# Optimization experiments

Measured on AMD Instinct MI355X. Metric: run time of the kernel, lower is better.

## Reference

```python
import jax, jax.numpy as jnp
import numpy as np

B, S, D, H = 2, 2048, 1024, 16
HD = D // H  # head dim = 64


def setup_inputs() -> dict:
    key = jax.random.key(0)
    ks = jax.random.split(key, 5)
    scale = 1.0 / np.sqrt(D)
    return {
        "hidden_states": jax.random.normal(ks[0], (B, S, D), jnp.float32),
        "attention_mask": jax.random.normal(ks[1], (B, 1, 1, S), jnp.float32),
        "Wq": jax.random.normal(ks[2], (D, D), jnp.float32) * scale,
        "bq": jnp.zeros((D,), jnp.float32),
        "Wk": jax.random.normal(ks[3], (D, D), jnp.float32) * scale,
        "bk": jnp.zeros((D,), jnp.float32),
        "Wv": jax.random.normal(ks[4], (D, D), jnp.float32) * scale,
        "bv": jnp.zeros((D,), jnp.float32),
    }


def _split_heads(x):
    # [B,S,D] -> [B,H,S,HD]
    return x.reshape(B, S, H, HD).transpose(0, 2, 1, 3)


def reference(hidden_states, attention_mask, Wq, bq, Wk, bk, Wv, bv):
    # torch Linear: y = x @ W.T + b
    q = _split_heads(hidden_states @ Wq.T + bq)
    k = _split_heads(hidden_states @ Wk.T + bk)
    v = _split_heads(hidden_states @ Wv.T + bv)

    scores = jnp.einsum("bhqd,bhkd->bhqk", q, k)
    # Faithful to source: with a mask present, the 1/sqrt(head_dim) scaling
    # is overwritten and raw scores are multiplied by the binary key mask.
    mask = (attention_mask >= 0).astype(scores.dtype)  # [B,1,1,S]
    probs = scores * mask
    # dropout prob = 0 (eval) -> identity

    ctx = jnp.einsum("bhqk,bhkd->bhqd", probs, v)
    ctx = ctx.transpose(0, 2, 1, 3).reshape(B, S, D)
    return ctx
```

## Files before the change

### kernel.cpp

```cpp
#include <hip/hip_runtime.h>

#define BB 2
#define SS 2048
#define DD 1024
#define HH 16
#define HDIM 64
#define MTOT 4096

typedef unsigned short u16;
typedef __bf16 bf16_t;
typedef bf16_t bf16x8 __attribute__((ext_vector_type(8)));
typedef float floatx4 __attribute__((ext_vector_type(4)));
typedef float floatx16 __attribute__((ext_vector_type(16)));

__device__ __forceinline__ float bf2f(u16 u) {
  union { unsigned int i; float f; } x;
  x.i = ((unsigned int)u) << 16;
  return x.f;
}
__device__ __forceinline__ u16 f2bf(float f) {
  union { float f; unsigned int i; } x;
  x.f = f;
  unsigned int r = x.i + 0x7fffu + ((x.i >> 16) & 1u);
  return (u16)(r >> 16);
}

__device__ __forceinline__ void gload16(const u16* g, u16* l) {
  __builtin_amdgcn_global_load_lds(
      (const __attribute__((address_space(1))) unsigned int*)g,
      (__attribute__((address_space(3))) unsigned int*)l, 16, 0, 0);
}

__global__ __launch_bounds__(256) void cast_to_bf16(
    const float* __restrict__ hs, const float* __restrict__ wq,
    const float* __restrict__ wk, const float* __restrict__ wv,
    u16* __restrict__ hs_b, u16* __restrict__ wq_b,
    u16* __restrict__ wk_b, u16* __restrict__ wv_b) {
  int fid = blockIdx.x * 256 + threadIdx.x;
  const float* src;
  u16* dst;
  int local;
  if (fid < 1048576) { src = hs; dst = hs_b; local = fid; }
  else if (fid < 1310720) { src = wq; dst = wq_b; local = fid - 1048576; }
  else if (fid < 1572864) { src = wk; dst = wk_b; local = fid - 1310720; }
  else { src = wv; dst = wv_b; local = fid - 1572864; }
  float4 v = reinterpret_cast<const float4*>(src)[local];
  ushort4 o;
  o.x = f2bf(v.x); o.y = f2bf(v.y); o.z = f2bf(v.z); o.w = f2bf(v.w);
  reinterpret_cast<ushort4*>(dst)[local] = o;
}

#define BKK 32
__global__ __launch_bounds__(256) void qkv_gemm_kernel(
    const u16* __restrict__ A,
    const u16* __restrict__ Wq, const u16* __restrict__ Wk, const u16* __restrict__ Wv,
    const float* __restrict__ bq, const float* __restrict__ bk, const float* __restrict__ bv,
    u16* __restrict__ Qo, u16* __restrict__ Ko, u16* __restrict__ Vo) {
  __shared__ u16 sA[128 * BKK];
  __shared__ u16 sB[128 * BKK];
  const int mt = blockIdx.y, ntall = blockIdx.x;
  const int seg = ntall >> 3, nt = ntall & 7;
  const u16* Wp = (seg == 0) ? Wq : (seg == 1) ? Wk : Wv;
  const float* bp = (seg == 0) ? bq : (seg == 1) ? bk : bv;
  u16* Out = (seg == 0) ? Qo : (seg == 1) ? Ko : Vo;
  const int m0 = mt * 128, n0 = nt * 128;
  const int tid = threadIdx.x;
  const int lane = tid & 63, wave = tid >> 6;
  const int wm = (wave >> 1) * 64, wn = (wave & 1) * 64;
  const int l32 = lane & 31, khalf = lane >> 5;
  const int srow0 = wave * 32 + (lane >> 2);
  const int scol = (lane & 3) * 8;
  floatx16 acc[2][2] = {};
  for (int k0 = 0; k0 < DD; k0 += BKK) {
#pragma unroll
    for (int c = 0; c < 2; ++c) {
      int r = srow0 + c * 16;
      gload16(A + (size_t)(m0 + r) * DD + k0 + scol, sA + r * BKK + scol);
      gload16(Wp + (size_t)(n0 + r) * DD + k0 + scol, sB + r * BKK + scol);
    }
    __syncthreads();
#pragma unroll
    for (int kk = 0; kk < 2; ++kk) {
      bf16x8 af[2], bfr[2];
#pragma unroll
      for (int i = 0; i < 2; ++i)
        af[i] = *reinterpret_cast<const bf16x8*>(sA + (wm + i * 32 + l32) * BKK + kk * 16 + khalf * 8);
#pragma unroll
      for (int j = 0; j < 2; ++j)
        bfr[j] = *reinterpret_cast<const bf16x8*>(sB + (wn + j * 32 + l32) * BKK + kk * 16 + khalf * 8);
#pragma unroll
      for (int i = 0; i < 2; ++i)
#pragma unroll
        for (int j = 0; j < 2; ++j)
          acc[i][j] = __builtin_amdgcn_mfma_f32_32x32x16_bf16(af[i], bfr[j], acc[i][j], 0, 0, 0);
    }
    __syncthreads();
  }
#pragma unroll
  for (int j = 0; j < 2; ++j) {
    int col = n0 + wn + j * 32 + l32;
    float bias = bp[col];
#pragma unroll
    for (int i = 0; i < 2; ++i) {
#pragma unroll
      for (int reg = 0; reg < 16; ++reg) {
        int row = m0 + wm + i * 32 + (reg & 3) + 8 * (reg >> 2) + 4 * khalf;
        Out[(size_t)row * DD + col] = f2bf(acc[i][j][reg] + bias);
      }
    }
  }
}

__global__ __launch_bounds__(256) void m_partial_kernel(
    const u16* __restrict__ Xb, const u16* __restrict__ Yb,
    const float* __restrict__ am, float* __restrict__ mpart) {
  __shared__ float sX[64 * 68];
  __shared__ float sY[64 * 68];
  const int bh = blockIdx.y;
  const int b = bh >> 4, h = bh & 15;
  const int tid = threadIdx.x;
  const int e0 = (tid & 15) * 4, d0 = (tid >> 4) * 4;
  const int s0 = blockIdx.x * 64;
  float acc[4][4] = {};
#pragma unroll
  for (int c = 0; c < 2; ++c) {
    int L = tid + c * 256;
    int srow = L >> 3;
    int col = (L & 7) * 8;
    size_t g = (size_t)(b * SS + s0 + srow) * DD + h * HDIM + col;
    uint4 xraw = *reinterpret_cast<const uint4*>(Xb + g);
    uint4 yraw = *reinterpret_cast<const uint4*>(Yb + g);
    float m = (am[b * SS + s0 + srow] >= 0.f) ? 1.f : 0.f;
    unsigned int xw[4] = {xraw.x, xraw.y, xraw.z, xraw.w};
    unsigned int yw[4] = {yraw.x, yraw.y, yraw.z, yraw.w};
#pragma unroll
    for (int q = 0; q < 4; ++q) {
      sX[srow * 68 + col + 2 * q]     = m * bf2f((u16)(xw[q] & 0xffffu));
      sX[srow * 68 + col + 2 * q + 1] = m * bf2f((u16)(xw[q] >> 16));
      sY[srow * 68 + col + 2 * q]     = bf2f((u16)(yw[q] & 0xffffu));
      sY[srow * 68 + col + 2 * q + 1] = bf2f((u16)(yw[q] >> 16));
    }
  }
  __syncthreads();
  for (int s = 0; s < 64; ++s) {
    float4 xx = *reinterpret_cast<const float4*>(&sX[s * 68 + e0]);
    float4 yy = *reinterpret_cast<const float4*>(&sY[s * 68 + d0]);
    float xa[4] = {xx.x, xx.y, xx.z, xx.w};
    float ya[4] = {yy.x, yy.y, yy.z, yy.w};
#pragma unroll
    for (int i = 0; i < 4; ++i)
#pragma unroll
      for (int j = 0; j < 4; ++j) acc[i][j] += xa[i] * ya[j];
  }
  float* outp = mpart + ((size_t)(blockIdx.x * 32 + bh)) * 4096;
#pragma unroll
  for (int i = 0; i < 4; ++i) {
    float4 o = {acc[i][0], acc[i][1], acc[i][2], acc[i][3]};
    *reinterpret_cast<float4*>(&outp[(e0 + i) * 64 + d0]) = o;
  }
}

__global__ __launch_bounds__(128) void m_reduce_kernel(
    const float* __restrict__ mpart, u16* __restrict__ Mb) {
  int t = blockIdx.x * 128 + threadIdx.x;
  const float* p = mpart + (size_t)t * 4;
  float4 s = {0.f, 0.f, 0.f, 0.f};
#pragma unroll
  for (int pc = 0; pc < 32; ++pc) {
    float4 v = *reinterpret_cast<const float4*>(p + (size_t)pc * 131072);
    s.x += v.x; s.y += v.y; s.z += v.z; s.w += v.w;
  }
  ushort4 o = {f2bf(s.x), f2bf(s.y), f2bf(s.z), f2bf(s.w)};
  *reinterpret_cast<ushort4*>(Mb + (size_t)t * 4) = o;
}

__global__ __launch_bounds__(256) void ctx_kernel(
    const u16* __restrict__ Qb, const u16* __restrict__ Mb, float* __restrict__ Out) {
  __shared__ u16 sMT[64 * 72];
  const int m0 = blockIdx.x * 128;
  const int h = blockIdx.y;
  const int b = m0 >> 11;
  const int bh = b * HH + h;
  const int tid = threadIdx.x;
  const u16* mg = Mb + (size_t)bh * 4096;
#pragma unroll
  for (int c = 0; c < 2; ++c) {
    int L = c * 256 + tid;
    int d = L >> 3, e = (L & 7) * 8;
    *reinterpret_cast<uint4*>(&sMT[d * 72 + e]) =
        *reinterpret_cast<const uint4*>(&mg[d * 64 + e]);
  }
  __syncthreads();
  const int lane = tid & 63, wave = tid >> 6;
  const int l32 = lane & 31, khalf = lane >> 5;
  const int arow = m0 + wave * 32 + l32;
  const u16* qrow = Qb + (size_t)arow * DD + h * HDIM + khalf * 8;
  bf16x8 af[4], bfr[2][4];
#pragma unroll
  for (int k0 = 0; k0 < 4; ++k0) {
    af[k0] = *reinterpret_cast<const bf16x8*>(qrow + k0 * 16);
#pragma unroll
    for (int j = 0; j < 2; ++j)
      bfr[j][k0] = *reinterpret_cast<const bf16x8*>(
          &sMT[(j * 32 + l32) * 72 + k0 * 16 + khalf * 8]);
  }
  floatx16 acc[2] = {};
#pragma unroll
  for (int j = 0; j < 2; ++j)
#pragma unroll
    for (int k0 = 0; k0 < 4; ++k0)
      acc[j] = __builtin_amdgcn_mfma_f32_32x32x16_bf16(af[k0], bfr[j][k0], acc[j], 0, 0, 0);
#pragma unroll
  for (int j = 0; j < 2; ++j) {
    int col = h * HDIM + j * 32 + l32;
#pragma unroll
    for (int reg = 0; reg < 16; ++reg) {
      int r = m0 + wave * 32 + (reg & 3) + 8 * (reg >> 2) + 4 * khalf;
      Out[(size_t)r * DD + col] = acc[j][reg];
    }
  }
}

extern "C" void kernel_launch(void* const* d_in, const int* in_sizes, int n_in,
                              void* d_out, int out_size, void* d_ws, size_t ws_size,
                              hipStream_t stream) {
  const float* hs = (const float*)d_in[0];
  const float* am = (const float*)d_in[1];
  const float* wq = (const float*)d_in[2];
  const float* bq = (const float*)d_in[3];
  const float* wk = (const float*)d_in[4];
  const float* bk = (const float*)d_in[5];
  const float* wv = (const float*)d_in[6];
  const float* bv = (const float*)d_in[7];
  float* out = (float*)d_out;
  char* ws = (char*)d_ws;

  u16* hs_b = (u16*)(ws);
  u16* wq_b = (u16*)(ws + 8388608);
  u16* wk_b = (u16*)(ws + 10485760);
  u16* wv_b = (u16*)(ws + 12582912);
  u16* q_b  = (u16*)(ws + 14680064);
  u16* k_b  = (u16*)(ws + 23068672);
  u16* v_b  = (u16*)(ws + 31457280);
  float* mpart = (float*)(ws + 39845888);
  u16* m_b  = (u16*)(ws + 56623104);

  cast_to_bf16<<<7168, 256, 0, stream>>>(hs, wq, wk, wv, hs_b, wq_b, wk_b, wv_b);
  qkv_gemm_kernel<<<dim3(24, 32), 256, 0, stream>>>(hs_b, wq_b, wk_b, wv_b,
                                                    bq, bk, bv, q_b, k_b, v_b);
  m_partial_kernel<<<dim3(32, 32), 256, 0, stream>>>(v_b, k_b, am, mpart);
  m_reduce_kernel<<<256, 128, 0, stream>>>(mpart, m_b);
  ctx_kernel<<<dim3(32, 16), 256, 0, stream>>>(q_b, m_b, out);
}
```

Baseline: 147.5 us.

## Pipeline QKV GEMM with triple-buffered async LDS loads and swizzled layout

Rewrites the QKV projection GEMM to use BK=64 tiles in a three-stage LDS ring buffer, issuing global-to-LDS loads two stages ahead and waiting with explicit vmcnt counters, so memory latency overlaps MFMA work. It also XOR-swizzles the LDS layout to avoid bank conflicts and moves to 512-thread blocks with 8 waves, each computing a 64x32 subtile. The cost is more shared memory (96KB per block) and hand-managed wait counts that must match the number of outstanding loads.

```diff
diff --git a/kernel.cpp b/kernel.cpp
--- a/kernel.cpp
+++ b/kernel.cpp
@@ -50,63 +50,83 @@
   reinterpret_cast<ushort4*>(dst)[local] = o;
 }
 
-#define BKK 32
-__global__ __launch_bounds__(256) void qkv_gemm_kernel(
+__global__ __launch_bounds__(512, 2) void qkv_gemm_p3(
     const u16* __restrict__ A,
     const u16* __restrict__ Wq, const u16* __restrict__ Wk, const u16* __restrict__ Wv,
     const float* __restrict__ bq, const float* __restrict__ bk, const float* __restrict__ bv,
     u16* __restrict__ Qo, u16* __restrict__ Ko, u16* __restrict__ Vo) {
-  __shared__ u16 sA[128 * BKK];
-  __shared__ u16 sB[128 * BKK];
-  const int mt = blockIdx.y, ntall = blockIdx.x;
-  const int seg = ntall >> 3, nt = ntall & 7;
+  __shared__ u16 sA[3][128 * 64];
+  __shared__ u16 sB[3][128 * 64];
+  const int id = blockIdx.x;
+  const int seg = id >> 8, rem = id & 255;
+  const int mt = rem >> 3, nt = rem & 7;
   const u16* Wp = (seg == 0) ? Wq : (seg == 1) ? Wk : Wv;
   const float* bp = (seg == 0) ? bq : (seg == 1) ? bk : bv;
   u16* Out = (seg == 0) ? Qo : (seg == 1) ? Ko : Vo;
   const int m0 = mt * 128, n0 = nt * 128;
   const int tid = threadIdx.x;
   const int lane = tid & 63, wave = tid >> 6;
-  const int wm = (wave >> 1) * 64, wn = (wave & 1) * 64;
   const int l32 = lane & 31, khalf = lane >> 5;
-  const int srow0 = wave * 32 + (lane >> 2);
-  const int scol = (lane & 3) * 8;
-  floatx16 acc[2][2] = {};
-  for (int k0 = 0; k0 < DD; k0 += BKK) {
-#pragma unroll
-    for (int c = 0; c < 2; ++c) {
-      int r = srow0 + c * 16;
-      gload16(A + (size_t)(m0 + r) * DD + k0 + scol, sA + r * BKK + scol);
-      gload16(Wp + (size_t)(n0 + r) * DD + k0 + scol, sB + r * BKK + scol);
-    }
-    __syncthreads();
-#pragma unroll
-    for (int kk = 0; kk < 2; ++kk) {
-      bf16x8 af[2], bfr[2];
-#pragma unroll
-      for (int i = 0; i < 2; ++i)
-        af[i] = *reinterpret_cast<const bf16x8*>(sA + (wm + i * 32 + l32) * BKK + kk * 16 + khalf * 8);
-#pragma unroll
-      for (int j = 0; j < 2; ++j)
-        bfr[j] = *reinterpret_cast<const bf16x8*>(sB + (wn + j * 32 + l32) * BKK + kk * 16 + khalf * 8);
-#pragma unroll
-      for (int i = 0; i < 2; ++i)
-#pragma unroll
-        for (int j = 0; j < 2; ++j)
-          acc[i][j] = __builtin_amdgcn_mfma_f32_32x32x16_bf16(af[i], bfr[j], acc[i][j], 0, 0, 0);
-    }
-    __syncthreads();
-  }
-#pragma unroll
-  for (int j = 0; j < 2; ++j) {
-    int col = n0 + wn + j * 32 + l32;
-    float bias = bp[col];
-#pragma unroll
-    for (int i = 0; i < 2; ++i) {
-#pragma unroll
-      for (int reg = 0; reg < 16; ++reg) {
-        int row = m0 + wm + i * 32 + (reg & 3) + 8 * (reg >> 2) + 4 * khalf;
-        Out[(size_t)row * DD + col] = f2bf(acc[i][j][reg] + bias);
-      }
+  const int wm = (wave >> 2) * 64;
+  const int wn = (wave & 3) * 32;
+
+  int srow[2], sgc[2], soff[2];
+#pragma unroll
+  for (int c = 0; c < 2; ++c) {
+    int L = c * 512 + tid;
+    srow[c] = L >> 3;
+    sgc[c] = ((L & 7) ^ (srow[c] & 7)) << 3;
+    soff[c] = L << 3;
+  }
+
+#define STAGE(buf, kbase)                                                  \
+  {                                                                        \
+    _Pragma("unroll") for (int c = 0; c < 2; ++c) {                        \
+      gload16(A + (size_t)(m0 + srow[c]) * DD + (kbase) + sgc[c],          \
+              &sA[buf][soff[c]]);                                          \
+      gload16(Wp + (size_t)(n0 + srow[c]) * DD + (kbase) + sgc[c],         \
+              &sB[buf][soff[c]]);                                          \
+    }                                                                      \
+  }
+
+  floatx16 acc[2] = {};
+  STAGE(0, 0);
+  STAGE(1, 64);
+  asm volatile("s_waitcnt vmcnt(4)" ::: "memory");
+  __builtin_amdgcn_s_barrier();
+
+  int cur = 0;
+  for (int t = 0; t < 16; ++t) {
+    if (t < 14) {
+      const int nb = (cur >= 1) ? cur - 1 : 2;
+      STAGE(nb, (t + 2) * 64);
+    }
+    const u16* pA = sA[cur];
+    const u16* pB = sB[cur];
+#pragma unroll
+    for (int ks = 0; ks < 4; ++ks) {
+      const int sw = (((ks * 2 + khalf) ^ (l32 & 7)) << 3);
+      bf16x8 b = *reinterpret_cast<const bf16x8*>(pB + (wn + l32) * 64 + sw);
+      bf16x8 a0 = *reinterpret_cast<const bf16x8*>(pA + (wm + l32) * 64 + sw);
+      bf16x8 a1 = *reinterpret_cast<const bf16x8*>(pA + (wm + 32 + l32) * 64 + sw);
+      acc[0] = __builtin_amdgcn_mfma_f32_32x32x16_bf16(a0, b, acc[0], 0, 0, 0);
+      acc[1] = __builtin_amdgcn_mfma_f32_32x32x16_bf16(a1, b, acc[1], 0, 0, 0);
+    }
+    if (t < 14) asm volatile("s_waitcnt vmcnt(4)" ::: "memory");
+    else if (t == 14) asm volatile("s_waitcnt vmcnt(0)" ::: "memory");
+    if (t < 15) __builtin_amdgcn_s_barrier();
+    cur = (cur < 2) ? cur + 1 : 0;
+  }
+#undef STAGE
+
+  const int col = n0 + wn + l32;
+  const float bias = bp[col];
+#pragma unroll
+  for (int i = 0; i < 2; ++i) {
+#pragma unroll
+    for (int reg = 0; reg < 16; ++reg) {
+      int row = m0 + wm + i * 32 + (reg & 3) + 8 * (reg >> 2) + 4 * khalf;
+      Out[(size_t)row * DD + col] = f2bf(acc[i][reg] + bias);
     }
   }
 }
@@ -246,8 +266,8 @@
   u16* m_b  = (u16*)(ws + 56623104);
 
   cast_to_bf16<<<7168, 256, 0, stream>>>(hs, wq, wk, wv, hs_b, wq_b, wk_b, wv_b);
-  qkv_gemm_kernel<<<dim3(24, 32), 256, 0, stream>>>(hs_b, wq_b, wk_b, wv_b,
-                                                    bq, bk, bv, q_b, k_b, v_b);
+  qkv_gemm_p3<<<768, 512, 0, stream>>>(hs_b, wq_b, wk_b, wv_b,
+                                       bq, bk, bv, q_b, k_b, v_b);
   m_partial_kernel<<<dim3(32, 32), 256, 0, stream>>>(v_b, k_b, am, mpart);
   m_reduce_kernel<<<256, 128, 0, stream>>>(mpart, m_b);
   ctx_kernel<<<dim3(32, 16), 256, 0, stream>>>(q_b, m_b, out);
```

New measurement: 162.9 us. 10.5% more time.

## Widen GEMM K-tile with XOR-swizzled LDS and fuse M reduction into ctx kernel

Applied to the files above, without the earlier changes.

The QKV GEMM now stages K=64 per iteration instead of 32, and uses an XOR swizzle on the LDS column index to avoid bank conflicts. That halves the number of barrier round-trips. Each m_partial block now processes two 64-row chunks, which halves the partial count to 16. The separate m_reduce kernel is removed: ctx_kernel sums the 16 partials directly while loading M into shared memory. This drops one launch and the bf16 M buffer, at the cost of each ctx block redundantly reducing partials (32 blocks per head repeat the same sum).

```diff
diff --git a/kernel.cpp b/kernel.cpp
--- a/kernel.cpp
+++ b/kernel.cpp
@@ -50,7 +50,7 @@
   reinterpret_cast<ushort4*>(dst)[local] = o;
 }
 
-#define BKK 32
+#define BKK 64
 __global__ __launch_bounds__(256) void qkv_gemm_kernel(
     const u16* __restrict__ A,
     const u16* __restrict__ Wq, const u16* __restrict__ Wk, const u16* __restrict__ Wv,
@@ -68,26 +68,32 @@
   const int lane = tid & 63, wave = tid >> 6;
   const int wm = (wave >> 1) * 64, wn = (wave & 1) * 64;
   const int l32 = lane & 31, khalf = lane >> 5;
-  const int srow0 = wave * 32 + (lane >> 2);
-  const int scol = (lane & 3) * 8;
+  int srow[4], sgc[4], soff[4];
+#pragma unroll
+  for (int c = 0; c < 4; ++c) {
+    int L = c * 256 + tid;
+    srow[c] = L >> 3;
+    sgc[c] = ((L & 7) ^ (srow[c] & 7)) << 3;
+    soff[c] = L << 3;
+  }
   floatx16 acc[2][2] = {};
   for (int k0 = 0; k0 < DD; k0 += BKK) {
 #pragma unroll
-    for (int c = 0; c < 2; ++c) {
-      int r = srow0 + c * 16;
-      gload16(A + (size_t)(m0 + r) * DD + k0 + scol, sA + r * BKK + scol);
-      gload16(Wp + (size_t)(n0 + r) * DD + k0 + scol, sB + r * BKK + scol);
+    for (int c = 0; c < 4; ++c) {
+      gload16(A + (size_t)(m0 + srow[c]) * DD + k0 + sgc[c], sA + soff[c]);
+      gload16(Wp + (size_t)(n0 + srow[c]) * DD + k0 + sgc[c], sB + soff[c]);
     }
     __syncthreads();
 #pragma unroll
-    for (int kk = 0; kk < 2; ++kk) {
+    for (int kk = 0; kk < 4; ++kk) {
+      const int sw = ((kk * 2 + khalf) ^ (l32 & 7)) << 3;
       bf16x8 af[2], bfr[2];
 #pragma unroll
       for (int i = 0; i < 2; ++i)
-        af[i] = *reinterpret_cast<const bf16x8*>(sA + (wm + i * 32 + l32) * BKK + kk * 16 + khalf * 8);
+        af[i] = *reinterpret_cast<const bf16x8*>(sA + (wm + i * 32 + l32) * BKK + sw);
 #pragma unroll
       for (int j = 0; j < 2; ++j)
-        bfr[j] = *reinterpret_cast<const bf16x8*>(sB + (wn + j * 32 + l32) * BKK + kk * 16 + khalf * 8);
+        bfr[j] = *reinterpret_cast<const bf16x8*>(sB + (wn + j * 32 + l32) * BKK + sw);
 #pragma unroll
       for (int i = 0; i < 2; ++i)
 #pragma unroll
@@ -120,37 +126,40 @@
   const int b = bh >> 4, h = bh & 15;
   const int tid = threadIdx.x;
   const int e0 = (tid & 15) * 4, d0 = (tid >> 4) * 4;
-  const int s0 = blockIdx.x * 64;
   float acc[4][4] = {};
-#pragma unroll
-  for (int c = 0; c < 2; ++c) {
-    int L = tid + c * 256;
-    int srow = L >> 3;
-    int col = (L & 7) * 8;
-    size_t g = (size_t)(b * SS + s0 + srow) * DD + h * HDIM + col;
-    uint4 xraw = *reinterpret_cast<const uint4*>(Xb + g);
-    uint4 yraw = *reinterpret_cast<const uint4*>(Yb + g);
-    float m = (am[b * SS + s0 + srow] >= 0.f) ? 1.f : 0.f;
-    unsigned int xw[4] = {xraw.x, xraw.y, xraw.z, xraw.w};
-    unsigned int yw[4] = {yraw.x, yraw.y, yraw.z, yraw.w};
-#pragma unroll
-    for (int q = 0; q < 4; ++q) {
-      sX[srow * 68 + col + 2 * q]     = m * bf2f((u16)(xw[q] & 0xffffu));
-      sX[srow * 68 + col + 2 * q + 1] = m * bf2f((u16)(xw[q] >> 16));
-      sY[srow * 68 + col + 2 * q]     = bf2f((u16)(yw[q] & 0xffffu));
-      sY[srow * 68 + col + 2 * q + 1] = bf2f((u16)(yw[q] >> 16));
-    }
-  }
-  __syncthreads();
-  for (int s = 0; s < 64; ++s) {
-    float4 xx = *reinterpret_cast<const float4*>(&sX[s * 68 + e0]);
-    float4 yy = *reinterpret_cast<const float4*>(&sY[s * 68 + d0]);
-    float xa[4] = {xx.x, xx.y, xx.z, xx.w};
-    float ya[4] = {yy.x, yy.y, yy.z, yy.w};
-#pragma unroll
-    for (int i = 0; i < 4; ++i)
-#pragma unroll
-      for (int j = 0; j < 4; ++j) acc[i][j] += xa[i] * ya[j];
+  for (int cs = 0; cs < 2; ++cs) {
+    const int s0 = (blockIdx.x * 2 + cs) * 64;
+    if (cs) __syncthreads();
+#pragma unroll
+    for (int c = 0; c < 2; ++c) {
+      int L = tid + c * 256;
+      int srow = L >> 3;
+      int col = (L & 7) * 8;
+      size_t g = (size_t)(b * SS + s0 + srow) * DD + h * HDIM + col;
+      uint4 xraw = *reinterpret_cast<const uint4*>(Xb + g);
+      uint4 yraw = *reinterpret_cast<const uint4*>(Yb + g);
+      float m = (am[b * SS + s0 + srow] >= 0.f) ? 1.f : 0.f;
+      unsigned int xw[4] = {xraw.x, xraw.y, xraw.z, xraw.w};
+      unsigned int yw[4] = {yraw.x, yraw.y, yraw.z, yraw.w};
+#pragma unroll
+      for (int q = 0; q < 4; ++q) {
+        sX[srow * 68 + col + 2 * q]     = m * bf2f((u16)(xw[q] & 0xffffu));
+        sX[srow * 68 + col + 2 * q + 1] = m * bf2f((u16)(xw[q] >> 16));
+        sY[srow * 68 + col + 2 * q]     = bf2f((u16)(yw[q] & 0xffffu));
+        sY[srow * 68 + col + 2 * q + 1] = bf2f((u16)(yw[q] >> 16));
+      }
+    }
+    __syncthreads();
+    for (int s = 0; s < 64; ++s) {
+      float4 xx = *reinterpret_cast<const float4*>(&sX[s * 68 + e0]);
+      float4 yy = *reinterpret_cast<const float4*>(&sY[s * 68 + d0]);
+      float xa[4] = {xx.x, xx.y, xx.z, xx.w};
+      float ya[4] = {yy.x, yy.y, yy.z, yy.w};
+#pragma unroll
+      for (int i = 0; i < 4; ++i)
+#pragma unroll
+        for (int j = 0; j < 4; ++j) acc[i][j] += xa[i] * ya[j];
+    }
   }
   float* outp = mpart + ((size_t)(blockIdx.x * 32 + bh)) * 4096;
 #pragma unroll
@@ -160,35 +169,27 @@
   }
 }
 
-__global__ __launch_bounds__(128) void m_reduce_kernel(
-    const float* __restrict__ mpart, u16* __restrict__ Mb) {
-  int t = blockIdx.x * 128 + threadIdx.x;
-  const float* p = mpart + (size_t)t * 4;
-  float4 s = {0.f, 0.f, 0.f, 0.f};
-#pragma unroll
-  for (int pc = 0; pc < 32; ++pc) {
-    float4 v = *reinterpret_cast<const float4*>(p + (size_t)pc * 131072);
-    s.x += v.x; s.y += v.y; s.z += v.z; s.w += v.w;
-  }
-  ushort4 o = {f2bf(s.x), f2bf(s.y), f2bf(s.z), f2bf(s.w)};
-  *reinterpret_cast<ushort4*>(Mb + (size_t)t * 4) = o;
-}
-
 __global__ __launch_bounds__(256) void ctx_kernel(
-    const u16* __restrict__ Qb, const u16* __restrict__ Mb, float* __restrict__ Out) {
+    const u16* __restrict__ Qb, const float* __restrict__ mpart, float* __restrict__ Out) {
   __shared__ u16 sMT[64 * 72];
   const int m0 = blockIdx.x * 128;
   const int h = blockIdx.y;
   const int b = m0 >> 11;
   const int bh = b * HH + h;
   const int tid = threadIdx.x;
-  const u16* mg = Mb + (size_t)bh * 4096;
-#pragma unroll
-  for (int c = 0; c < 2; ++c) {
-    int L = c * 256 + tid;
-    int d = L >> 3, e = (L & 7) * 8;
-    *reinterpret_cast<uint4*>(&sMT[d * 72 + e]) =
-        *reinterpret_cast<const uint4*>(&mg[d * 64 + e]);
+#pragma unroll
+  for (int c = 0; c < 4; ++c) {
+    int L4 = c * 256 + tid;
+    float4 s = {0.f, 0.f, 0.f, 0.f};
+#pragma unroll
+    for (int pc = 0; pc < 16; ++pc) {
+      const float4* p4 = reinterpret_cast<const float4*>(mpart + ((size_t)(pc * 32 + bh)) * 4096);
+      float4 t = p4[L4];
+      s.x += t.x; s.y += t.y; s.z += t.z; s.w += t.w;
+    }
+    int d = L4 >> 4, e = (L4 & 15) * 4;
+    ushort4 o = {f2bf(s.x), f2bf(s.y), f2bf(s.z), f2bf(s.w)};
+    *reinterpret_cast<ushort4*>(&sMT[d * 72 + e]) = o;
   }
   __syncthreads();
   const int lane = tid & 63, wave = tid >> 6;
@@ -243,12 +244,10 @@
   u16* k_b  = (u16*)(ws + 23068672);
   u16* v_b  = (u16*)(ws + 31457280);
   float* mpart = (float*)(ws + 39845888);
-  u16* m_b  = (u16*)(ws + 56623104);
 
   cast_to_bf16<<<7168, 256, 0, stream>>>(hs, wq, wk, wv, hs_b, wq_b, wk_b, wv_b);
   qkv_gemm_kernel<<<dim3(24, 32), 256, 0, stream>>>(hs_b, wq_b, wk_b, wv_b,
                                                     bq, bk, bv, q_b, k_b, v_b);
-  m_partial_kernel<<<dim3(32, 32), 256, 0, stream>>>(v_b, k_b, am, mpart);
-  m_reduce_kernel<<<256, 128, 0, stream>>>(mpart, m_b);
-  ctx_kernel<<<dim3(32, 16), 256, 0, stream>>>(q_b, m_b, out);
-}
+  m_partial_kernel<<<dim3(16, 32), 256, 0, stream>>>(v_b, k_b, am, mpart);
+  ctx_kernel<<<dim3(32, 16), 256, 0, stream>>>(q_b, mpart, out);
+}
```

Result: slower. 153.5 us (+4.1%).
